# Optimization experiments

Hardware: AMD Instinct MI355X
Metric: run time of the kernel (lower is better)

The kernel has to match this reference:

```python
import jax, jax.numpy as jnp
import numpy as np

B, T, D, H = 32, 4096, 512, 8
HD = D // H
SCALE = HD ** -0.5


def setup_inputs() -> dict:
    key = jax.random.key(0)
    ks = jax.random.split(key, 5)
    s = 0.02
    return {
        "enc": jax.random.normal(ks[0], (B, T, D), dtype=jnp.float32),
        "Wq": jax.random.normal(ks[1], (D, D), dtype=jnp.float32) * s,
        "Wk": jax.random.normal(ks[2], (D, D), dtype=jnp.float32) * s,
        "Wv": jax.random.normal(ks[3], (D, D), dtype=jnp.float32) * s,
        "Wo": jax.random.normal(ks[4], (D, D), dtype=jnp.float32) * s,
    }


def reference(enc, Wq, Wk, Wv, Wo):
    b, t, d = enc.shape
    # projections (torch Linear: y = x @ W.T)
    q = enc[:, -1, :] @ Wq.T                     # [B, D]
    k = (enc @ Wk.T).reshape(b, t, H, HD)        # [B, T, H, HD]
    v = (enc @ Wv.T).reshape(b, t, H, HD)        # [B, T, H, HD]
    q = q.reshape(b, H, HD)                      # [B, H, HD]
    scores = jnp.einsum('bhd,bthd->bht', q, k) * SCALE   # [B, H, T]
    weights = jax.nn.softmax(scores, axis=-1)             # [B, H, T]
    context = jnp.einsum('bht,bthd->bhd', weights, v)     # [B, H, HD]
    context = context.reshape(b, d) @ Wo.T                # [B, D]
    return (context, weights.mean(axis=1))
```

## Files before the change

### kernel.cpp

```cpp
#include <hip/hip_runtime.h>

#define BB 32
#define TT 4096
#define DD 512
#define HH 8
#define HDD 64
#define SCALE_F 0.125f
#define CHUNKS 32
#define TC 128
#define TILE 32
#define NT (TC / TILE)

__global__ __launch_bounds__(256) void k_qu(const float* __restrict__ enc,
                                            const float* __restrict__ Wq,
                                            const float* __restrict__ Wk,
                                            float* __restrict__ u) {
    __shared__ float x[DD];
    __shared__ float qh[HDD];
    int b = blockIdx.x >> 3, h = blockIdx.x & 7;
    int tid = threadIdx.x;
    const float* el = enc + ((size_t)b * TT + (TT - 1)) * DD;
    for (int i = tid; i < DD; i += 256) x[i] = el[i];
    __syncthreads();
    if (tid < HDD) {
        const float4* wr = (const float4*)(Wq + (size_t)(h * HDD + tid) * DD);
        float acc = 0.f;
#pragma unroll 4
        for (int d = 0; d < DD / 4; ++d) {
            float4 w = wr[d];
            acc += w.x * x[4 * d] + w.y * x[4 * d + 1] + w.z * x[4 * d + 2] + w.w * x[4 * d + 3];
        }
        qh[tid] = acc;
    }
    __syncthreads();
#pragma unroll
    for (int k = 0; k < 2; ++k) {
        int d = tid + 256 * k;
        float acc = 0.f;
#pragma unroll 8
        for (int j = 0; j < HDD; ++j)
            acc += qh[j] * Wk[(size_t)(h * HDD + j) * DD + d];
        u[(size_t)(b * HH + h) * DD + d] = acc * SCALE_F;
    }
}

__global__ __launch_bounds__(256) void k_main(const float* __restrict__ enc,
                                              const float* __restrict__ u,
                                              float* __restrict__ wt,
                                              float* __restrict__ lsum,
                                              float* __restrict__ partial) {
    __shared__ float et[TILE * DD];
    __shared__ float stile[TILE][HH];
    int b = blockIdx.x / CHUNKS, c = blockIdx.x % CHUNKS;
    int t0 = c * TC;
    int tid = threadIdx.x, wave = tid >> 6, lane = tid & 63;

    const float* ub = u + (size_t)b * HH * DD;
    float4 uA[HH], uB[HH];
#pragma unroll
    for (int h = 0; h < HH; ++h) {
        uA[h] = *(const float4*)(ub + h * DD + 4 * lane);
        uB[h] = *(const float4*)(ub + h * DD + 256 + 4 * lane);
    }
    bool b3 = (lane & 8) != 0, b4 = (lane & 16) != 0, b5 = (lane & 32) != 0;
    int myh = ((lane >> 3) & 1) * 4 + ((lane >> 4) & 1) * 2 + ((lane >> 5) & 1);

    float Lacc = 0.f;
    float2 acc[HH];
#pragma unroll
    for (int h = 0; h < HH; ++h) acc[h] = make_float2(0.f, 0.f);
    int d0 = tid * 2;

    for (int tile = 0; tile < NT; ++tile) {
        int tb = t0 + tile * TILE;
        const float4* gp = (const float4*)(enc + (size_t)(b * TT + tb) * DD);
        float4* lp = (float4*)et;
#pragma unroll
        for (int k = 0; k < 16; ++k) {
            int idx = tid + 256 * k;
            lp[idx] = gp[idx];
        }
        __syncthreads();
        for (int tt = wave; tt < TILE; tt += 4) {
            const float* row = et + tt * DD;
            float4 e0 = *(const float4*)(row + 4 * lane);
            float4 e1 = *(const float4*)(row + 256 + 4 * lane);
            float a[HH];
#pragma unroll
            for (int h = 0; h < HH; ++h)
                a[h] = uA[h].x * e0.x + uA[h].y * e0.y + uA[h].z * e0.z + uA[h].w * e0.w
                     + uB[h].x * e1.x + uB[h].y * e1.y + uB[h].z * e1.z + uB[h].w * e1.w;
            float s[4];
#pragma unroll
            for (int j = 0; j < 4; ++j) {
                float snd = b3 ? a[j] : a[j + 4];
                float kp  = b3 ? a[j + 4] : a[j];
                s[j] = kp + __shfl_xor(snd, 8, 64);
            }
            float p[2];
#pragma unroll
            for (int j = 0; j < 2; ++j) {
                float snd = b4 ? s[j] : s[j + 2];
                float kp  = b4 ? s[j + 2] : s[j];
                p[j] = kp + __shfl_xor(snd, 16, 64);
            }
            float snd = b5 ? p[0] : p[1];
            float q0 = (b5 ? p[1] : p[0]) + __shfl_xor(snd, 32, 64);
            q0 += __shfl_xor(q0, 1, 64);
            q0 += __shfl_xor(q0, 2, 64);
            q0 += __shfl_xor(q0, 4, 64);
            if ((lane & 7) == 0) stile[tt][myh] = __expf(q0);
        }
        __syncthreads();
        {
            int h = tid >> 5, ttv = tid & 31;
            wt[(size_t)(b * HH + h) * TT + tb + ttv] = stile[ttv][h];
        }
        if (tid < HH) {
#pragma unroll
            for (int t = 0; t < TILE; ++t) Lacc += stile[t][tid];
        }
#pragma unroll 4
        for (int r = 0; r < TILE; ++r) {
            float2 e = *(const float2*)(et + r * DD + d0);
            const float4* sp = (const float4*)stile[r];
            float4 w0 = sp[0], w1 = sp[1];
            acc[0].x += w0.x * e.x; acc[0].y += w0.x * e.y;
            acc[1].x += w0.y * e.x; acc[1].y += w0.y * e.y;
            acc[2].x += w0.z * e.x; acc[2].y += w0.z * e.y;
            acc[3].x += w0.w * e.x; acc[3].y += w0.w * e.y;
            acc[4].x += w1.x * e.x; acc[4].y += w1.x * e.y;
            acc[5].x += w1.y * e.x; acc[5].y += w1.y * e.y;
            acc[6].x += w1.z * e.x; acc[6].y += w1.z * e.y;
            acc[7].x += w1.w * e.x; acc[7].y += w1.w * e.y;
        }
        __syncthreads();
    }
    float* pp = partial + (size_t)(b * CHUNKS + c) * HH * DD + d0;
#pragma unroll
    for (int h = 0; h < HH; ++h) *(float2*)(pp + h * DD) = acc[h];
    if (tid < HH) lsum[(size_t)(b * CHUNKS + c) * HH + tid] = Lacc;
}

__global__ __launch_bounds__(256) void k_vctx(const float* __restrict__ partial,
                                              const float* __restrict__ lsum,
                                              const float* __restrict__ Wv,
                                              float* __restrict__ ctxv) {
    __shared__ float cs[DD];
    __shared__ float Linv;
    int b = blockIdx.x >> 3, h = blockIdx.x & 7;
    int tid = threadIdx.x;
    if (tid == 0) {
        float L = 0.f;
#pragma unroll 8
        for (int c = 0; c < CHUNKS; ++c) L += lsum[(size_t)(b * CHUNKS + c) * HH + h];
        Linv = 1.0f / L;
    }
    float a0 = 0.f, a1 = 0.f;
    const float* pb = partial + (size_t)(b * CHUNKS) * HH * DD + (size_t)h * DD;
#pragma unroll 8
    for (int c = 0; c < CHUNKS; ++c) {
        const float* pp = pb + (size_t)c * HH * DD;
        a0 += pp[tid]; a1 += pp[tid + 256];
    }
    __syncthreads();
    cs[tid] = a0 * Linv; cs[tid + 256] = a1 * Linv;
    __syncthreads();
    int out = tid >> 2, q = tid & 3;
    int i = h * HDD + out;
    const float4* wr = (const float4*)(Wv + (size_t)i * DD + q * 128);
    const float* cc = cs + q * 128;
    float acc = 0.f;
#pragma unroll 8
    for (int d = 0; d < 32; ++d) {
        float4 w = wr[d];
        acc += w.x * cc[4 * d] + w.y * cc[4 * d + 1] + w.z * cc[4 * d + 2] + w.w * cc[4 * d + 3];
    }
    acc += __shfl_xor(acc, 1, 64);
    acc += __shfl_xor(acc, 2, 64);
    if (q == 0) ctxv[(size_t)b * DD + i] = acc;
}

__global__ __launch_bounds__(256) void k_o(const float* __restrict__ ctxv,
                                           const float* __restrict__ Wo,
                                           float* __restrict__ out0) {
    __shared__ float cs[DD];
    int b = blockIdx.x >> 3, g = blockIdx.x & 7;
    int tid = threadIdx.x;
    for (int i = tid; i < DD; i += 256) cs[i] = ctxv[(size_t)b * DD + i];
    __syncthreads();
    int out = tid >> 2, q = tid & 3;
    int o = g * HDD + out;
    const float4* wr = (const float4*)(Wo + (size_t)o * DD + q * 128);
    const float* cc = cs + q * 128;
    float acc = 0.f;
#pragma unroll 8
    for (int d = 0; d < 32; ++d) {
        float4 w = wr[d];
        acc += w.x * cc[4 * d] + w.y * cc[4 * d + 1] + w.z * cc[4 * d + 2] + w.w * cc[4 * d + 3];
    }
    acc += __shfl_xor(acc, 1, 64);
    acc += __shfl_xor(acc, 2, 64);
    if (q == 0) out0[(size_t)b * DD + o] = acc;
}

__global__ __launch_bounds__(256) void k_out1(const float* __restrict__ wt,
                                              const float* __restrict__ lsum,
                                              float* __restrict__ out1) {
    __shared__ float Linv[HH];
    int b = blockIdx.x >> 3, seg = blockIdx.x & 7;
    int tid = threadIdx.x;
    if (tid < HH) {
        float s = 0.f;
#pragma unroll 8
        for (int c = 0; c < CHUNKS; ++c) s += lsum[(size_t)(b * CHUNKS + c) * HH + tid];
        Linv[tid] = 0.125f / s;
    }
    __syncthreads();
#pragma unroll
    for (int k = 0; k < 2; ++k) {
        int t = seg * 512 + tid + 256 * k;
        float s = 0.f;
#pragma unroll
        for (int h = 0; h < HH; ++h)
            s += wt[(size_t)(b * HH + h) * TT + t] * Linv[h];
        out1[(size_t)b * TT + t] = s;
    }
}

extern "C" void kernel_launch(void* const* d_in, const int* in_sizes, int n_in,
                              void* d_out, int out_size, void* d_ws, size_t ws_size,
                              hipStream_t stream) {
    const float* enc = (const float*)d_in[0];
    const float* Wq  = (const float*)d_in[1];
    const float* Wk  = (const float*)d_in[2];
    const float* Wv  = (const float*)d_in[3];
    const float* Wo  = (const float*)d_in[4];

    float* ws = (float*)d_ws;
    float* u       = ws;
    float* wt      = u + (size_t)BB * HH * DD;
    float* lsum    = wt + (size_t)BB * HH * TT;
    float* partial = lsum + (size_t)BB * CHUNKS * HH;
    float* ctxv    = partial + (size_t)BB * CHUNKS * HH * DD;

    float* out0 = (float*)d_out;
    float* out1 = out0 + BB * DD;

    hipLaunchKernelGGL(k_qu,    dim3(BB * HH),     dim3(256), 0, stream, enc, Wq, Wk, u);
    hipLaunchKernelGGL(k_main,  dim3(BB * CHUNKS), dim3(256), 0, stream, enc, u, wt, lsum, partial);
    hipLaunchKernelGGL(k_vctx,  dim3(BB * HH),     dim3(256), 0, stream, partial, lsum, Wv, ctxv);
    hipLaunchKernelGGL(k_o,     dim3(BB * HH),     dim3(256), 0, stream, ctxv, Wo, out0);
    hipLaunchKernelGGL(k_out1,  dim3(BB * HH),     dim3(256), 0, stream, wt, lsum, out1);
}
```

Baseline: 416.5 us.

## Stream enc rows per wave from registers with prefetch, drop shared tile staging

The main kernel no longer stages 32-row tiles of enc through shared memory with block barriers. Each wave now owns 64 contiguous rows, loads them straight from global memory into registers with a two-row prefetch, and accumulates the weighted sums for all heads in registers using shuffles to broadcast the weights. Per-wave partial sums are combined once at the end through a shared reduction buffer, and the chunk count is halved so each block covers 256 rows. In exchange, register pressure rises (64 accumulator floats plus the u vectors), which may lower occupancy, and fewer blocks are launched.

```diff
diff --git a/kernel.cpp b/kernel.cpp
--- a/kernel.cpp
+++ b/kernel.cpp
@@ -6,10 +6,9 @@
 #define HH 8
 #define HDD 64
 #define SCALE_F 0.125f
-#define CHUNKS 32
-#define TC 128
-#define TILE 32
-#define NT (TC / TILE)
+#define CHUNKS 16
+#define TC 256
+#define RW 64
 
 __global__ __launch_bounds__(256) void k_qu(const float* __restrict__ enc,
                                             const float* __restrict__ Wq,
@@ -49,11 +48,13 @@
                                               float* __restrict__ wt,
                                               float* __restrict__ lsum,
                                               float* __restrict__ partial) {
-    __shared__ float et[TILE * DD];
-    __shared__ float stile[TILE][HH];
+    __shared__ float red[4][HH][DD];
+    __shared__ float ls[HH];
     int b = blockIdx.x / CHUNKS, c = blockIdx.x % CHUNKS;
     int t0 = c * TC;
     int tid = threadIdx.x, wave = tid >> 6, lane = tid & 63;
+    if (tid < HH) ls[tid] = 0.f;
+    __syncthreads();
 
     const float* ub = u + (size_t)b * HH * DD;
     float4 uA[HH], uB[HH];
@@ -65,81 +66,100 @@
     bool b3 = (lane & 8) != 0, b4 = (lane & 16) != 0, b5 = (lane & 32) != 0;
     int myh = ((lane >> 3) & 1) * 4 + ((lane >> 4) & 1) * 2 + ((lane >> 5) & 1);
 
+    float4 accA[HH], accB[HH];
+#pragma unroll
+    for (int h = 0; h < HH; ++h) {
+        accA[h] = make_float4(0.f, 0.f, 0.f, 0.f);
+        accB[h] = make_float4(0.f, 0.f, 0.f, 0.f);
+    }
+
+    int trow = t0 + wave * RW;
+    const float* rp = enc + ((size_t)b * TT + trow) * DD;
+    float* wrow = wt + (size_t)(b * HH + myh) * TT + trow;
+
+    float4 c0 = *(const float4*)(rp + 4 * lane);
+    float4 c1 = *(const float4*)(rp + 256 + 4 * lane);
+    float4 d0 = *(const float4*)(rp + DD + 4 * lane);
+    float4 d1 = *(const float4*)(rp + DD + 256 + 4 * lane);
     float Lacc = 0.f;
-    float2 acc[HH];
-#pragma unroll
-    for (int h = 0; h < HH; ++h) acc[h] = make_float2(0.f, 0.f);
-    int d0 = tid * 2;
-
-    for (int tile = 0; tile < NT; ++tile) {
-        int tb = t0 + tile * TILE;
-        const float4* gp = (const float4*)(enc + (size_t)(b * TT + tb) * DD);
-        float4* lp = (float4*)et;
-#pragma unroll
-        for (int k = 0; k < 16; ++k) {
-            int idx = tid + 256 * k;
-            lp[idx] = gp[idx];
-        }
-        __syncthreads();
-        for (int tt = wave; tt < TILE; tt += 4) {
-            const float* row = et + tt * DD;
-            float4 e0 = *(const float4*)(row + 4 * lane);
-            float4 e1 = *(const float4*)(row + 256 + 4 * lane);
-            float a[HH];
-#pragma unroll
-            for (int h = 0; h < HH; ++h)
-                a[h] = uA[h].x * e0.x + uA[h].y * e0.y + uA[h].z * e0.z + uA[h].w * e0.w
-                     + uB[h].x * e1.x + uB[h].y * e1.y + uB[h].z * e1.z + uB[h].w * e1.w;
-            float s[4];
-#pragma unroll
-            for (int j = 0; j < 4; ++j) {
-                float snd = b3 ? a[j] : a[j + 4];
-                float kp  = b3 ? a[j + 4] : a[j];
-                s[j] = kp + __shfl_xor(snd, 8, 64);
-            }
-            float p[2];
-#pragma unroll
-            for (int j = 0; j < 2; ++j) {
-                float snd = b4 ? s[j] : s[j + 2];
-                float kp  = b4 ? s[j + 2] : s[j];
-                p[j] = kp + __shfl_xor(snd, 16, 64);
-            }
-            float snd = b5 ? p[0] : p[1];
-            float q0 = (b5 ? p[1] : p[0]) + __shfl_xor(snd, 32, 64);
-            q0 += __shfl_xor(q0, 1, 64);
-            q0 += __shfl_xor(q0, 2, 64);
-            q0 += __shfl_xor(q0, 4, 64);
-            if ((lane & 7) == 0) stile[tt][myh] = __expf(q0);
-        }
-        __syncthreads();
-        {
-            int h = tid >> 5, ttv = tid & 31;
-            wt[(size_t)(b * HH + h) * TT + tb + ttv] = stile[ttv][h];
-        }
-        if (tid < HH) {
-#pragma unroll
-            for (int t = 0; t < TILE; ++t) Lacc += stile[t][tid];
-        }
-#pragma unroll 4
-        for (int r = 0; r < TILE; ++r) {
-            float2 e = *(const float2*)(et + r * DD + d0);
-            const float4* sp = (const float4*)stile[r];
-            float4 w0 = sp[0], w1 = sp[1];
-            acc[0].x += w0.x * e.x; acc[0].y += w0.x * e.y;
-            acc[1].x += w0.y * e.x; acc[1].y += w0.y * e.y;
-            acc[2].x += w0.z * e.x; acc[2].y += w0.z * e.y;
-            acc[3].x += w0.w * e.x; acc[3].y += w0.w * e.y;
-            acc[4].x += w1.x * e.x; acc[4].y += w1.x * e.y;
-            acc[5].x += w1.y * e.x; acc[5].y += w1.y * e.y;
-            acc[6].x += w1.z * e.x; acc[6].y += w1.z * e.y;
-            acc[7].x += w1.w * e.x; acc[7].y += w1.w * e.y;
-        }
-        __syncthreads();
-    }
-    float* pp = partial + (size_t)(b * CHUNKS + c) * HH * DD + d0;
-#pragma unroll
-    for (int h = 0; h < HH; ++h) *(float2*)(pp + h * DD) = acc[h];
-    if (tid < HH) lsum[(size_t)(b * CHUNKS + c) * HH + tid] = Lacc;
+
+    for (int i = 0; i < RW; ++i) {
+        float4 e0 = c0, e1 = c1;
+        c0 = d0; c1 = d1;
+        if (i + 2 < RW) {
+            const float* np = rp + (size_t)(i + 2) * DD;
+            d0 = *(const float4*)(np + 4 * lane);
+            d1 = *(const float4*)(np + 256 + 4 * lane);
+        }
+        float a[HH];
+#pragma unroll
+        for (int h = 0; h < HH; ++h)
+            a[h] = uA[h].x * e0.x + uA[h].y * e0.y + uA[h].z * e0.z + uA[h].w * e0.w
+                 + uB[h].x * e1.x + uB[h].y * e1.y + uB[h].z * e1.z + uB[h].w * e1.w;
+        float s[4];
+#pragma unroll
+        for (int j = 0; j < 4; ++j) {
+            float snd = b3 ? a[j] : a[j + 4];
+            float kp  = b3 ? a[j + 4] : a[j];
+            s[j] = kp + __shfl_xor(snd, 8, 64);
+        }
+        float p[2];
+#pragma unroll
+        for (int j = 0; j < 2; ++j) {
+            float snd = b4 ? s[j] : s[j + 2];
+            float kp  = b4 ? s[j + 2] : s[j];
+            p[j] = kp + __shfl_xor(snd, 16, 64);
+        }
+        float snd = b5 ? p[0] : p[1];
+        float q0 = (b5 ? p[1] : p[0]) + __shfl_xor(snd, 32, 64);
+        q0 += __shfl_xor(q0, 1, 64);
+        q0 += __shfl_xor(q0, 2, 64);
+        q0 += __shfl_xor(q0, 4, 64);
+        float w = __expf(q0);
+        Lacc += w;
+        if ((lane & 7) == 0) wrow[i] = w;
+        float wv[HH];
+        wv[0] = __shfl(w, 0, 64);
+        wv[1] = __shfl(w, 32, 64);
+        wv[2] = __shfl(w, 16, 64);
+        wv[3] = __shfl(w, 48, 64);
+        wv[4] = __shfl(w, 8, 64);
+        wv[5] = __shfl(w, 40, 64);
+        wv[6] = __shfl(w, 24, 64);
+        wv[7] = __shfl(w, 56, 64);
+#pragma unroll
+        for (int h = 0; h < HH; ++h) {
+            accA[h].x += wv[h] * e0.x; accA[h].y += wv[h] * e0.y;
+            accA[h].z += wv[h] * e0.z; accA[h].w += wv[h] * e0.w;
+            accB[h].x += wv[h] * e1.x; accB[h].y += wv[h] * e1.y;
+            accB[h].z += wv[h] * e1.z; accB[h].w += wv[h] * e1.w;
+        }
+    }
+
+#pragma unroll
+    for (int h = 0; h < HH; ++h) {
+        *(float4*)&red[wave][h][4 * lane] = accA[h];
+        *(float4*)&red[wave][h][256 + 4 * lane] = accB[h];
+    }
+    if ((lane & 7) == 0) atomicAdd(&ls[myh], Lacc);
+    __syncthreads();
+    {
+        int h = tid >> 5, col = (tid & 31) * 4;
+        float* pb = partial + ((size_t)(b * CHUNKS + c) * HH + h) * DD;
+#pragma unroll
+        for (int j = 0; j < 4; ++j) {
+            float4 r0 = *(const float4*)&red[0][h][col + 128 * j];
+            float4 r1 = *(const float4*)&red[1][h][col + 128 * j];
+            float4 r2 = *(const float4*)&red[2][h][col + 128 * j];
+            float4 r3 = *(const float4*)&red[3][h][col + 128 * j];
+            float4 o = make_float4(r0.x + r1.x + r2.x + r3.x,
+                                   r0.y + r1.y + r2.y + r3.y,
+                                   r0.z + r1.z + r2.z + r3.z,
+                                   r0.w + r1.w + r2.w + r3.w);
+            *(float4*)(pb + col + 128 * j) = o;
+        }
+    }
+    if (tid < HH) lsum[(size_t)(b * CHUNKS + c) * HH + tid] = ls[tid];
 }
 
 __global__ __launch_bounds__(256) void k_vctx(const float* __restrict__ partial,
```

Measured after the change: 409.0 us. Within noise of the previous version (-1.8%).
